# Kernel optimization log

Hardware: AMD Instinct MI355X
Metric: run time of the kernel (lower is better)

Reference implementation:

```python
import jax, jax.numpy as jnp
import numpy as np

N = 100000
E = 1600000
D_IN = 128
D_HID = 128
D_OUT = 16


def setup_inputs() -> dict:
    key = jax.random.key(0)
    ks = jax.random.split(key, 10)
    x = jax.random.normal(ks[0], (N, D_IN), dtype=jnp.float32)
    edge_index = jax.random.randint(ks[1], (2, E), 0, N, dtype=jnp.int32)
    s = 1.0 / np.sqrt(D_IN)
    sh = 1.0 / np.sqrt(D_HID)
    W1l = jax.random.uniform(ks[2], (D_HID, D_IN), jnp.float32, -s, s)
    b1l = jax.random.uniform(ks[3], (D_HID,), jnp.float32, -s, s)
    W1r = jax.random.uniform(ks[4], (D_HID, D_IN), jnp.float32, -s, s)
    W2l = jax.random.uniform(ks[5], (D_HID, D_HID), jnp.float32, -sh, sh)
    b2l = jax.random.uniform(ks[6], (D_HID,), jnp.float32, -sh, sh)
    W2r = jax.random.uniform(ks[7], (D_HID, D_HID), jnp.float32, -sh, sh)
    Wc = jax.random.uniform(ks[8], (D_OUT, D_HID), jnp.float32, -sh, sh)
    bc = jax.random.uniform(ks[9], (D_OUT,), jnp.float32, -sh, sh)
    return {"x": x, "edge_index": edge_index, "W1l": W1l, "b1l": b1l, "W1r": W1r,
            "W2l": W2l, "b2l": b2l, "W2r": W2r, "Wc": Wc, "bc": bc}


def _sage_conv(x, src, dst, Wl, bl, Wr):
    # PyG SAGEConv (mean aggr): out_i = Wl @ mean_{j in N(i)} x_j + bl + Wr @ x_i
    n = x.shape[0]
    msg = x[src]                                             # [E, d] gather
    summed = jax.ops.segment_sum(msg, dst, num_segments=n)   # [N, d] scatter-add
    cnt = jax.ops.segment_sum(jnp.ones((src.shape[0],), x.dtype), dst, num_segments=n)
    agg = summed / jnp.maximum(cnt, 1.0)[:, None]            # mean; isolated nodes -> 0
    return agg @ Wl.T + bl + x @ Wr.T


def reference(x, edge_index, W1l, b1l, W1r, W2l, b2l, W2r, Wc, bc):
    src, dst = edge_index[0], edge_index[1]
    h = jax.nn.relu(_sage_conv(x, src, dst, W1l, b1l, W1r))
    # dropout p=0.5 is identity at inference (training=False)
    z = _sage_conv(h, src, dst, W2l, b2l, W2r)
    return z @ Wc.T + bc
```

## Files before the change

### kernel.cpp

```cpp
#include <hip/hip_runtime.h>

#define BSHIFT 8
#define MAXB   512
#define BCAP   6912
#define CHUNK  4096

typedef __bf16 bf16x8 __attribute__((ext_vector_type(8)));
typedef float  f32x4  __attribute__((ext_vector_type(4)));
typedef float  f32x2  __attribute__((ext_vector_type(2)));

__device__ __forceinline__ unsigned short f2b(float f) {
  unsigned u = __float_as_uint(f);
  return (unsigned short)((u + 0x7fffu + ((u >> 16) & 1u)) >> 16);
}
__device__ __forceinline__ float b2f_lo(unsigned u) {
  return __uint_as_float(u << 16);
}
__device__ __forceinline__ float b2f_hi(unsigned u) {
  return __uint_as_float(u & 0xffff0000u);
}

__global__ __launch_bounds__(256) void k_front(
    const int* __restrict__ ei, int E, int* __restrict__ bcnt,
    unsigned* __restrict__ edg,
    const float* __restrict__ x, unsigned short* __restrict__ xb,
    unsigned* __restrict__ xq, int ngroups,
    const float* __restrict__ W1l, const float* __restrict__ W1r,
    unsigned short* __restrict__ Wb,
    const float* __restrict__ Wc, const float* __restrict__ bc,
    const float* __restrict__ W2l, const float* __restrict__ W2r,
    const float* __restrict__ b2, unsigned short* __restrict__ Mb,
    float* __restrict__ bias2,
    unsigned short* __restrict__ Pnb, int ZR, int nbin, int ncast) {
  __shared__ int lh[MAXB], lbase[MAXB], lcur[MAXB];
  __shared__ int ldst[CHUNK];
  const int b = blockIdx.x;
  const int t = threadIdx.x;
  if (b < nbin) {
    for (int i = t; i < MAXB; i += 256) { lh[i] = 0; lcur[i] = 0; }
    __syncthreads();
    const int e0 = b * CHUNK;
    const int n = min(E - e0, CHUNK);
    const int* __restrict__ src = ei;
    const int* __restrict__ dst = ei + E;
    for (int j = t; j < n; j += 256) {
      int d = dst[e0 + j];
      ldst[j] = d;
      atomicAdd(&lh[((unsigned)d) >> BSHIFT], 1);
    }
    __syncthreads();
    for (int i = t; i < MAXB; i += 256)
      if (lh[i]) lbase[i] = atomicAdd(&bcnt[i], lh[i]);
    __syncthreads();
    for (int j = t; j < n; j += 256) {
      int d = ldst[j];
      unsigned s = (unsigned)src[e0 + j];
      int bk = ((unsigned)d) >> BSHIFT;
      int p = lbase[bk] + atomicAdd(&lcur[bk], 1);
      if (p < BCAP) edg[(size_t)bk * BCAP + p] = ((unsigned)(d & 255) << 17) | s;
    }
  } else if (b < nbin + ncast) {
    int g = (b - nbin) * 256 + t;
    if (g < ngroups) {
      float4 v = ((const float4*)x)[g];
      ushort4 o;
      o.x = f2b(v.x); o.y = f2b(v.y); o.z = f2b(v.z); o.w = f2b(v.w);
      ((ushort4*)xb)[g] = o;
      int q8 = __builtin_amdgcn_cvt_pk_fp8_f32(v.x, v.y, 0, false);
      q8 = __builtin_amdgcn_cvt_pk_fp8_f32(v.z, v.w, q8, true);
      xq[g] = (unsigned)q8;
    }
  } else {
    int bb = b - nbin - ncast;
    if (bb < 128) {
      int idx = bb * 256 + t;
      int col = idx >> 8, k = idx & 255;
      float v = (k < 128) ? W1l[col * 128 + k] : W1r[col * 128 + (k - 128)];
      Wb[col * 256 + k] = f2b(v);
    } else if (bb < 144) {
      int mb = bb - 128;
      int mat = mb >> 3;
      const float* W2 = mat ? W2r : W2l;
      int o = (mb & 7) * 2 + (t >> 7);
      int k = t & 127;
      float s = 0.f;
      for (int j = 0; j < 128; ++j) s = fmaf(Wc[o * 128 + j], W2[j * 128 + k], s);
      Mb[(size_t)(mat * 16 + o) * 128 + k] = f2b(s);
      if (mb == 0 && t < 16) {
        float sb = bc[t];
        for (int j = 0; j < 128; ++j) sb = fmaf(Wc[t * 128 + j], b2[j], sb);
        bias2[t] = sb;
      }
    } else {
      if (t < 64) ((unsigned*)(xb + (size_t)ZR * 128))[t] = 0;
      if (t < 32) xq[(size_t)ZR * 32 + t] = 0;
      if (t < 8)  ((unsigned*)(Pnb + (size_t)ZR * 16))[t] = 0;
    }
  }
}

__global__ __launch_bounds__(1024) void k_build(
    const unsigned* __restrict__ edg, const int* __restrict__ bcnt,
    int* __restrict__ eidx, int* __restrict__ rowcnt, int N, int ZR) {
  __shared__ int lsrc[BCAP];
  __shared__ int lcnt[256], lstart[256], lcur[256];
  __shared__ int wsum[4];
  const int b = blockIdx.x;
  const int t = threadIdx.x;
  const int node0 = b << BSHIFT;
  const int nb = min(256, N - node0);
  const int ecount = min(bcnt[b], BCAP);
  const unsigned* __restrict__ ed = edg + (size_t)b * BCAP;
  if (t < 256) lcnt[t] = 0;
  __syncthreads();
  for (int j = t; j < ecount; j += 1024)
    atomicAdd(&lcnt[ed[j] >> 17], 1);
  __syncthreads();
  int incl = 0, pad = 0;
  if (t < 256) {
    int c = lcnt[t];
    pad = (c + 15) & ~15;
    incl = pad;
    int lane = t & 63;
#pragma unroll
    for (int off = 1; off < 64; off <<= 1) {
      int v = __shfl_up(incl, off, 64);
      if (lane >= off) incl += v;
    }
    if (lane == 63) wsum[t >> 6] = incl;
  }
  __syncthreads();
  if (t < 256) {
    int wv = t >> 6;
    int woff = 0;
    for (int i = 0; i < wv; ++i) woff += wsum[i];
    int excl = woff + incl - pad;
    lstart[t] = excl; lcur[t] = excl;
  }
  __syncthreads();
  for (int j = t; j < ecount; j += 1024) {
    unsigned e = ed[j];
    int p = atomicAdd(&lcur[e >> 17], 1);
    lsrc[p] = (int)(e & 0x1FFFFu);
  }
  if (t < 256) {
    int c = lcnt[t];
    int s0 = lstart[t] + c;
    int s1 = lstart[t] + ((c + 15) & ~15);
    for (int j = s0; j < s1; ++j) lsrc[j] = ZR;
  }
  __syncthreads();
  const int ebase = b * BCAP;
  int tot = wsum[0] + wsum[1] + wsum[2] + wsum[3];
  int ecountp = min(tot, BCAP);
  for (int j = 4 * t; j < ecountp; j += 4096) {
    int4 v = *(const int4*)&lsrc[j];
    *(int4*)&eidx[ebase + j] = v;
  }
  if (t < nb) {
    rowcnt[2 * (node0 + t)]     = ebase + lstart[t];
    rowcnt[2 * (node0 + t) + 1] = lcnt[t];
  }
}

__global__ __launch_bounds__(256) void k_agg1(
    const int* __restrict__ eidx, const int* __restrict__ rowcnt,
    const unsigned* __restrict__ xq, unsigned short* __restrict__ aggb, int N) {
  int wv = (blockIdx.x * 256 + threadIdx.x) >> 6;
  int lane = threadIdx.x & 63;
  const int sub = lane >> 4;
  const int li  = lane & 15;
  int n = wv * 4 + sub;
  const bool act = (n < N);
  int deg = 0;
  const int* el = eidx;
  if (act) {
    int2 rc = *(const int2*)(rowcnt + 2 * (size_t)n);
    deg = rc.y;
    el = eidx + rc.x;
  }
  f32x2 acc[4];
#pragma unroll
  for (int j = 0; j < 4; ++j) acc[j] = (f32x2){0.f, 0.f};

  for (int e = 0; e < deg; e += 4) {
    int4 q = *(const int4*)(el + e);
    uint2 v0 = *(const uint2*)(xq + (size_t)q.x * 32 + li * 2);
    uint2 v1 = *(const uint2*)(xq + (size_t)q.y * 32 + li * 2);
    uint2 v2 = *(const uint2*)(xq + (size_t)q.z * 32 + li * 2);
    uint2 v3 = *(const uint2*)(xq + (size_t)q.w * 32 + li * 2);
#define ADD8(v)                                                      \
    acc[0] += __builtin_amdgcn_cvt_pk_f32_fp8(v.x, false);           \
    acc[1] += __builtin_amdgcn_cvt_pk_f32_fp8(v.x, true);            \
    acc[2] += __builtin_amdgcn_cvt_pk_f32_fp8(v.y, false);           \
    acc[3] += __builtin_amdgcn_cvt_pk_f32_fp8(v.y, true);
    ADD8(v0) ADD8(v1) ADD8(v2) ADD8(v3)
#undef ADD8
  }
  if (act) {
    float sc = 1.0f / (float)max(deg, 1);
    uint4 o4;
    o4.x = (unsigned)f2b(acc[0].x * sc) | ((unsigned)f2b(acc[0].y * sc) << 16);
    o4.y = (unsigned)f2b(acc[1].x * sc) | ((unsigned)f2b(acc[1].y * sc) << 16);
    o4.z = (unsigned)f2b(acc[2].x * sc) | ((unsigned)f2b(acc[2].y * sc) << 16);
    o4.w = (unsigned)f2b(acc[3].x * sc) | ((unsigned)f2b(acc[3].y * sc) << 16);
    *(uint4*)(aggb + (size_t)n * 128 + li * 8) = o4;
  }
}

__global__ __launch_bounds__(256) void k_gemm1_mfma(
    const unsigned short* __restrict__ aggb, const unsigned short* __restrict__ xb,
    const unsigned short* __restrict__ Wb, const float* __restrict__ b1,
    const unsigned short* __restrict__ Mb,
    unsigned short* __restrict__ Pnb, float* __restrict__ Ps, int N) {
  __shared__ union {
    struct { unsigned short A[128 * 40]; unsigned short W[128 * 40]; } s;
    unsigned short H[128 * 136];
  } sm;
  const int t = threadIdx.x;
  const int w = t >> 6;
  const int lane = t & 63;
  const int q = lane >> 4;
  const int l16 = lane & 15;
  const int row0 = blockIdx.x * 128;

  f32x4 acc[2][8];
#pragma unroll
  for (int rt = 0; rt < 2; ++rt)
#pragma unroll
    for (int ct = 0; ct < 8; ++ct) acc[rt][ct] = (f32x4){0.f, 0.f, 0.f, 0.f};

  for (int kc = 0; kc < 8; ++kc) {
    const unsigned short* Asrc = (kc < 4) ? aggb : xb;
    const int koff = (kc & 3) * 32;
#pragma unroll
    for (int i = 0; i < 2; ++i) {
      int idx = t + i * 256;
      int row = idx >> 2, c4 = idx & 3;
      int gr = row0 + row; if (gr >= N) gr = N - 1;
      uint4 v = *(const uint4*)(Asrc + (size_t)gr * 128 + koff + c4 * 8);
      *(uint4*)(sm.s.A + row * 40 + c4 * 8) = v;
    }
#pragma unroll
    for (int i = 0; i < 2; ++i) {
      int idx = t + i * 256;
      int col = idx >> 2, c4 = idx & 3;
      uint4 v = *(const uint4*)(Wb + col * 256 + kc * 32 + c4 * 8);
      *(uint4*)(sm.s.W + col * 40 + c4 * 8) = v;
    }
    __syncthreads();
    bf16x8 afr[2];
#pragma unroll
    for (int rt = 0; rt < 2; ++rt)
      afr[rt] = *(const bf16x8*)(sm.s.A + (w * 32 + rt * 16 + l16) * 40 + q * 8);
    bf16x8 bfr[8];
#pragma unroll
    for (int ct = 0; ct < 8; ++ct)
      bfr[ct] = *(const bf16x8*)(sm.s.W + (ct * 16 + l16) * 40 + q * 8);
#pragma unroll
    for (int rt = 0; rt < 2; ++rt)
#pragma unroll
      for (int ct = 0; ct < 8; ++ct)
        acc[rt][ct] = __builtin_amdgcn_mfma_f32_16x16x32_bf16(
            afr[rt], bfr[ct], acc[rt][ct], 0, 0, 0);
    __syncthreads();
  }

  float bv[8];
#pragma unroll
  for (int ct = 0; ct < 8; ++ct) bv[ct] = b1[ct * 16 + l16];
#pragma unroll
  for (int rt = 0; rt < 2; ++rt) {
    int rl = w * 32 + rt * 16 + q * 4;
#pragma unroll
    for (int reg = 0; reg < 4; ++reg) {
#pragma unroll
      for (int ct = 0; ct < 8; ++ct) {
        float v = acc[rt][ct][reg] + bv[ct];
        sm.H[(rl + reg) * 136 + ct * 16 + l16] = f2b(v > 0.f ? v : 0.f);
      }
    }
  }
  __syncthreads();

  f32x4 acc2[2][2];
#pragma unroll
  for (int rt = 0; rt < 2; ++rt)
#pragma unroll
    for (int ct = 0; ct < 2; ++ct) acc2[rt][ct] = (f32x4){0.f, 0.f, 0.f, 0.f};
#pragma unroll
  for (int ks = 0; ks < 4; ++ks) {
    bf16x8 a2[2], b2v[2];
#pragma unroll
    for (int rt = 0; rt < 2; ++rt)
      a2[rt] = *(const bf16x8*)(sm.H + (w * 32 + rt * 16 + l16) * 136 + ks * 32 + q * 8);
#pragma unroll
    for (int ct = 0; ct < 2; ++ct)
      b2v[ct] = *(const bf16x8*)(Mb + (size_t)(ct * 16 + l16) * 128 + ks * 32 + q * 8);
#pragma unroll
    for (int rt = 0; rt < 2; ++rt)
#pragma unroll
      for (int ct = 0; ct < 2; ++ct)
        acc2[rt][ct] = __builtin_amdgcn_mfma_f32_16x16x32_bf16(
            a2[rt], b2v[ct], acc2[rt][ct], 0, 0, 0);
  }
#pragma unroll
  for (int rt = 0; rt < 2; ++rt) {
    int rbase = row0 + w * 32 + rt * 16 + q * 4;
#pragma unroll
    for (int reg = 0; reg < 4; ++reg) {
      int r = rbase + reg;
      Pnb[(size_t)r * 16 + l16] = f2b(acc2[rt][0][reg]);
      Ps[(size_t)r * 16 + l16] = acc2[rt][1][reg];
    }
  }
}

__global__ __launch_bounds__(256) void k_agg2_out(
    const int* __restrict__ eidx, const int* __restrict__ rowcnt,
    const unsigned short* __restrict__ Pnb, const float* __restrict__ Ps,
    const float* __restrict__ bias2, float* __restrict__ out, int N) {
  int i = (blockIdx.x * 256 + threadIdx.x) >> 6;
  int lane = threadIdx.x & 63;
  if (i >= N) return;
  const int sub = lane >> 2;
  const int li = lane & 3;
  int2 rc = *(const int2*)(rowcnt + 2 * (size_t)i);
  int deg = rc.y;
  const int* el = eidx + rc.x;
  f32x2 a0 = (f32x2){0.f, 0.f}, a1 = (f32x2){0.f, 0.f};
  for (int e = 0; e < deg; e += 16) {
    if (e + sub < deg) {
      int idx = el[e + sub];
      uint2 v = *(const uint2*)(Pnb + (size_t)idx * 16 + li * 4);
      a0 += (f32x2){b2f_lo(v.x), b2f_hi(v.x)};
      a1 += (f32x2){b2f_lo(v.y), b2f_hi(v.y)};
    }
  }
#pragma unroll
  for (int m = 4; m <= 32; m <<= 1) {
    a0.x += __shfl_xor(a0.x, m, 64);
    a0.y += __shfl_xor(a0.y, m, 64);
    a1.x += __shfl_xor(a1.x, m, 64);
    a1.y += __shfl_xor(a1.y, m, 64);
  }
  if (sub == 0) {
    float sc = 1.0f / (float)max(deg, 1);
    float4 self = *(const float4*)(Ps + (size_t)i * 16 + li * 4);
    float4 b = *(const float4*)(bias2 + li * 4);
    float4 o;
    o.x = a0.x * sc + self.x + b.x;
    o.y = a0.y * sc + self.y + b.y;
    o.z = a1.x * sc + self.z + b.z;
    o.w = a1.y * sc + self.w + b.w;
    *(float4*)(out + (size_t)i * 16 + li * 4) = o;
  }
}

extern "C" void kernel_launch(void* const* d_in, const int* in_sizes, int n_in,
                              void* d_out, int out_size, void* d_ws, size_t ws_size,
                              hipStream_t stream) {
  const float* x   = (const float*)d_in[0];
  const int*   ei  = (const int*)d_in[1];
  const float* W1l = (const float*)d_in[2];
  const float* b1l = (const float*)d_in[3];
  const float* W1r = (const float*)d_in[4];
  const float* W2l = (const float*)d_in[5];
  const float* b2l = (const float*)d_in[6];
  const float* W2r = (const float*)d_in[7];
  const float* Wc  = (const float*)d_in[8];
  const float* bc  = (const float*)d_in[9];
  float* out = (float*)d_out;

  const int N     = in_sizes[0] / 128;
  const int E     = in_sizes[1] / 2;
  const int Np    = ((N + 127) / 128) * 128;
  const int NBUCK = (N + 255) >> BSHIFT;
  const int ZR    = Np;
  const int NBIN  = (E + CHUNK - 1) / CHUNK;
  const int NCAST = (N * 32 + 255) / 256;

  char* ws = (char*)d_ws;
  size_t off = 0;
  auto alloc = [&](size_t bytes) {
    void* p = ws + off;
    off = (off + bytes + 255) & ~(size_t)255;
    return p;
  };
  int*            rowcnt   = (int*)           alloc((size_t)N * 8);
  int*            bcnt     = (int*)           alloc(MAXB * 4);
  unsigned*       edg      = (unsigned*)      alloc((size_t)NBUCK * BCAP * 4);
  int*            eidx     = (int*)           alloc((size_t)NBUCK * BCAP * 4);
  unsigned short* xb       = (unsigned short*)alloc((size_t)(Np + 1) * 128 * 2);
  unsigned*       xq       = (unsigned*)      alloc((size_t)(Np + 1) * 32 * 4);
  unsigned short* aggb     = (unsigned short*)alloc((size_t)Np * 128 * 2);
  unsigned short* Wb       = (unsigned short*)alloc((size_t)128 * 256 * 2);
  unsigned short* Mb       = (unsigned short*)alloc((size_t)32 * 128 * 2);
  unsigned short* Pnb      = (unsigned short*)alloc((size_t)(Np + 1) * 16 * 2);
  float*          Ps       = (float*)         alloc((size_t)Np * 16 * 4);
  float*          bias2    = (float*)         alloc(16 * 4);
  (void)ws_size; (void)n_in; (void)out_size;

  hipMemsetAsync(bcnt, 0, MAXB * 4, stream);
  k_front<<<NBIN + NCAST + 145, 256, 0, stream>>>(
      ei, E, bcnt, edg, x, xb, xq, N * 32,
      W1l, W1r, Wb, Wc, bc, W2l, W2r, b2l, Mb, bias2, Pnb, ZR, NBIN, NCAST);
  k_build<<<NBUCK, 1024, 0, stream>>>(edg, bcnt, eidx, rowcnt, N, ZR);
  k_agg1<<<(N + 15) / 16, 256, 0, stream>>>(eidx, rowcnt, xq, aggb, N);
  k_gemm1_mfma<<<Np / 128, 256, 0, stream>>>(aggb, xb, Wb, b1l, Mb, Pnb, Ps, N);
  k_agg2_out<<<(N + 3) / 4, 256, 0, stream>>>(eidx, rowcnt, Pnb, Ps, bias2, out, N);
}
```

Baseline: 239.1 us.

## Split cast from binning kernel, enlarge bin chunks, pad bucket counters

```diff
diff --git a/kernel.cpp b/kernel.cpp
--- a/kernel.cpp
+++ b/kernel.cpp
@@ -2,8 +2,9 @@
 
 #define BSHIFT 8
 #define MAXB   512
+#define BPAD   16
 #define BCAP   6912
-#define CHUNK  4096
+#define CHUNK  8192
 
 typedef __bf16 bf16x8 __attribute__((ext_vector_type(8)));
 typedef float  f32x4  __attribute__((ext_vector_type(4)));
@@ -20,58 +21,46 @@
   return __uint_as_float(u & 0xffff0000u);
 }
 
-__global__ __launch_bounds__(256) void k_front(
+__global__ __launch_bounds__(1024) void k_bin(
     const int* __restrict__ ei, int E, int* __restrict__ bcnt,
     unsigned* __restrict__ edg,
-    const float* __restrict__ x, unsigned short* __restrict__ xb,
-    unsigned* __restrict__ xq, int ngroups,
     const float* __restrict__ W1l, const float* __restrict__ W1r,
     unsigned short* __restrict__ Wb,
     const float* __restrict__ Wc, const float* __restrict__ bc,
     const float* __restrict__ W2l, const float* __restrict__ W2r,
     const float* __restrict__ b2, unsigned short* __restrict__ Mb,
     float* __restrict__ bias2,
-    unsigned short* __restrict__ Pnb, int ZR, int nbin, int ncast) {
+    unsigned short* __restrict__ xb, unsigned* __restrict__ xq,
+    unsigned short* __restrict__ Pnb, int ZR, int nbin) {
   __shared__ int lh[MAXB], lbase[MAXB], lcur[MAXB];
   __shared__ int ldst[CHUNK];
   const int b = blockIdx.x;
   const int t = threadIdx.x;
   if (b < nbin) {
-    for (int i = t; i < MAXB; i += 256) { lh[i] = 0; lcur[i] = 0; }
+    for (int i = t; i < MAXB; i += 1024) { lh[i] = 0; lcur[i] = 0; }
     __syncthreads();
     const int e0 = b * CHUNK;
     const int n = min(E - e0, CHUNK);
     const int* __restrict__ src = ei;
     const int* __restrict__ dst = ei + E;
-    for (int j = t; j < n; j += 256) {
+    for (int j = t; j < n; j += 1024) {
       int d = dst[e0 + j];
       ldst[j] = d;
       atomicAdd(&lh[((unsigned)d) >> BSHIFT], 1);
     }
     __syncthreads();
-    for (int i = t; i < MAXB; i += 256)
-      if (lh[i]) lbase[i] = atomicAdd(&bcnt[i], lh[i]);
+    for (int i = t; i < MAXB; i += 1024)
+      if (lh[i]) lbase[i] = atomicAdd(&bcnt[i * BPAD], lh[i]);
     __syncthreads();
-    for (int j = t; j < n; j += 256) {
+    for (int j = t; j < n; j += 1024) {
       int d = ldst[j];
       unsigned s = (unsigned)src[e0 + j];
       int bk = ((unsigned)d) >> BSHIFT;
       int p = lbase[bk] + atomicAdd(&lcur[bk], 1);
       if (p < BCAP) edg[(size_t)bk * BCAP + p] = ((unsigned)(d & 255) << 17) | s;
     }
-  } else if (b < nbin + ncast) {
-    int g = (b - nbin) * 256 + t;
-    if (g < ngroups) {
-      float4 v = ((const float4*)x)[g];
-      ushort4 o;
-      o.x = f2b(v.x); o.y = f2b(v.y); o.z = f2b(v.z); o.w = f2b(v.w);
-      ((ushort4*)xb)[g] = o;
-      int q8 = __builtin_amdgcn_cvt_pk_fp8_f32(v.x, v.y, 0, false);
-      q8 = __builtin_amdgcn_cvt_pk_fp8_f32(v.z, v.w, q8, true);
-      xq[g] = (unsigned)q8;
-    }
-  } else {
-    int bb = b - nbin - ncast;
+  } else if (t < 256) {
+    int bb = b - nbin;
     if (bb < 128) {
       int idx = bb * 256 + t;
       int col = idx >> 8, k = idx & 255;
@@ -99,6 +88,21 @@
   }
 }
 
+__global__ __launch_bounds__(256) void k_cast(
+    const float* __restrict__ x, unsigned short* __restrict__ xb,
+    unsigned* __restrict__ xq, int ngroups) {
+  int g = blockIdx.x * 256 + threadIdx.x;
+  if (g < ngroups) {
+    float4 v = ((const float4*)x)[g];
+    ushort4 o;
+    o.x = f2b(v.x); o.y = f2b(v.y); o.z = f2b(v.z); o.w = f2b(v.w);
+    ((ushort4*)xb)[g] = o;
+    int q8 = __builtin_amdgcn_cvt_pk_fp8_f32(v.x, v.y, 0, false);
+    q8 = __builtin_amdgcn_cvt_pk_fp8_f32(v.z, v.w, q8, true);
+    xq[g] = (unsigned)q8;
+  }
+}
+
 __global__ __launch_bounds__(1024) void k_build(
     const unsigned* __restrict__ edg, const int* __restrict__ bcnt,
     int* __restrict__ eidx, int* __restrict__ rowcnt, int N, int ZR) {
@@ -109,7 +113,7 @@
   const int t = threadIdx.x;
   const int node0 = b << BSHIFT;
   const int nb = min(256, N - node0);
-  const int ecount = min(bcnt[b], BCAP);
+  const int ecount = min(bcnt[b * BPAD], BCAP);
   const unsigned* __restrict__ ed = edg + (size_t)b * BCAP;
   if (t < 256) lcnt[t] = 0;
   __syncthreads();
@@ -388,7 +392,7 @@
     return p;
   };
   int*            rowcnt   = (int*)           alloc((size_t)N * 8);
-  int*            bcnt     = (int*)           alloc(MAXB * 4);
+  int*            bcnt     = (int*)           alloc((size_t)MAXB * BPAD * 4);
   unsigned*       edg      = (unsigned*)      alloc((size_t)NBUCK * BCAP * 4);
   int*            eidx     = (int*)           alloc((size_t)NBUCK * BCAP * 4);
   unsigned short* xb       = (unsigned short*)alloc((size_t)(Np + 1) * 128 * 2);
@@ -401,10 +405,11 @@
   float*          bias2    = (float*)         alloc(16 * 4);
   (void)ws_size; (void)n_in; (void)out_size;
 
-  hipMemsetAsync(bcnt, 0, MAXB * 4, stream);
-  k_front<<<NBIN + NCAST + 145, 256, 0, stream>>>(
-      ei, E, bcnt, edg, x, xb, xq, N * 32,
-      W1l, W1r, Wb, Wc, bc, W2l, W2r, b2l, Mb, bias2, Pnb, ZR, NBIN, NCAST);
+  hipMemsetAsync(bcnt, 0, (size_t)MAXB * BPAD * 4, stream);
+  k_bin<<<NBIN + 145, 1024, 0, stream>>>(
+      ei, E, bcnt, edg,
+      W1l, W1r, Wb, Wc, bc, W2l, W2r, b2l, Mb, bias2, xb, xq, Pnb, ZR, NBIN);
+  k_cast<<<NCAST, 256, 0, stream>>>(x, xb, xq, N * 32);
   k_build<<<NBUCK, 1024, 0, stream>>>(edg, bcnt, eidx, rowcnt, N, ZR);
   k_agg1<<<(N + 15) / 16, 256, 0, stream>>>(eidx, rowcnt, xq, aggb, N);
   k_gemm1_mfma<<<Np / 128, 256, 0, stream>>>(aggb, xb, Wb, b1l, Mb, Pnb, Ps, N);
```

New measurement: 236.5 us. Within noise of the previous version (-1.1%).
